# Kernel tuning notes

Hardware: AMD Instinct MI355X
Metric: run time of the kernel (lower is better)

Reference implementation:

```python
import jax, jax.numpy as jnp
import numpy as np

B, S, H, E, TOP_K = 4, 2048, 1024, 16, 4


def setup_inputs() -> dict:
    key = jax.random.key(0)
    ks = jax.random.split(key, 12)
    sc = 1.0 / np.sqrt(H)
    inp = {
        "x": jax.random.normal(ks[0], (B, S, H), dtype=jnp.float32),
        "image": jax.random.normal(ks[1], (B, S, H), dtype=jnp.float32),
        "text": jax.random.normal(ks[2], (B, S, H), dtype=jnp.float32),
        "audio": jax.random.normal(ks[3], (B, S, H), dtype=jnp.float32),
        # generalized router linear
        "Wg": jax.random.uniform(ks[4], (H, E), jnp.float32, -sc, sc),
        "bg": jax.random.uniform(ks[5], (E,), jnp.float32, -sc, sc),
        # per-modality router linears
        "Wi": jax.random.uniform(ks[6], (H, E), jnp.float32, -sc, sc),
        "bi": jax.random.uniform(ks[7], (E,), jnp.float32, -sc, sc),
        "Wt": jax.random.uniform(ks[8], (H, E), jnp.float32, -sc, sc),
        "bt": jax.random.uniform(ks[9], (E,), jnp.float32, -sc, sc),
        "Wa": jax.random.uniform(ks[10], (H, E), jnp.float32, -sc, sc),
        "ba": jax.random.uniform(ks[11], (E,), jnp.float32, -sc, sc),
    }
    return inp


def reference(x, image, text, audio, Wg, bg, Wi, bi, Wt, bt, Wa, ba):
    # combined_logits = generalized_router(x) + sum_m modality_router_m(modality_m)
    logits = (
        jnp.einsum("bsh,he->bse", x, Wg) + bg
        + jnp.einsum("bsh,he->bse", image, Wi) + bi
        + jnp.einsum("bsh,he->bse", text, Wt) + bt
        + jnp.einsum("bsh,he->bse", audio, Wa) + ba
    )  # [B,S,E]
    router_probs = jax.nn.softmax(logits, axis=-1)
    top_k_probs, top_k_indices = jax.lax.top_k(router_probs, TOP_K)
    top_k_probs = top_k_probs / jnp.sum(top_k_probs, axis=-1, keepdims=True)
    prob_per_expert = jnp.mean(router_probs, axis=(0, 1))  # [E]
    aux_loss = jnp.sum(prob_per_expert * jnp.log(prob_per_expert * E + 1e-9))
    return (top_k_indices, top_k_probs, aux_loss)
```

## Files before the change

kernel.cpp:

```cpp
#include <hip/hip_runtime.h>
#include <math.h>

constexpr int kTokens = 8192;
constexpr int kH      = 1024;
constexpr int kE      = 16;
constexpr int kTopK   = 4;
constexpr int kNC     = 16;

__global__ __launch_bounds__(128, 5)
void router_fmac(const float* __restrict__ x,   const float* __restrict__ img,
                 const float* __restrict__ txt, const float* __restrict__ aud,
                 const float* __restrict__ Wg,  const float* __restrict__ Wi,
                 const float* __restrict__ Wt,  const float* __restrict__ Wa,
                 float* __restrict__ partials)
{
    __shared__ float smem[2 * 2560];

    const int t   = threadIdx.x;
    const int bid = blockIdx.x;
    const int ks  = bid & 15;
    const int tg  = bid >> 4;
    const int m   = ks >> 2;
    const int k0  = (ks & 3) * 256;
    const int tok0 = tg * 128;

    const float* Xm = (m == 0) ? x  : (m == 1) ? img : (m == 2) ? txt : aud;
    const float* Wm = (m == 0) ? Wg : (m == 1) ? Wi  : (m == 2) ? Wt  : Wa;

    const int sc = t & 3;
    const int sr = t >> 2;

    float4 pf[4];

    {
        const float* src = Xm + (size_t)(tok0 + sr) * kH + k0 + sc * 4;
#pragma unroll
        for (int it = 0; it < 4; ++it)
            pf[it] = *(const float4*)(src + (size_t)(it * 32) * kH);
#pragma unroll
        for (int it = 0; it < 4; ++it)
            *(float4*)&smem[(sr + it * 32) * 20 + sc * 4] = pf[it];
    }
    __syncthreads();

    double dacc[kE];
#pragma unroll
    for (int e = 0; e < kE; ++e) dacc[e] = 0.0;
    float facc[kE];

    for (int p = 0; p < 16; ++p) {
        if (p < 15) {
            const float* src = Xm + (size_t)(tok0 + sr) * kH + k0 + (p + 1) * 16 + sc * 4;
#pragma unroll
            for (int it = 0; it < 4; ++it)
                pf[it] = *(const float4*)(src + (size_t)(it * 32) * kH);
        }

        if ((p & 3) == 0) {
#pragma unroll
            for (int e = 0; e < kE; ++e) facc[e] = 0.f;
        }

        const float* buf = smem + (p & 1) * 2560;
        float4 xv[4];
#pragma unroll
        for (int j4 = 0; j4 < 4; ++j4)
            xv[j4] = *(const float4*)&buf[t * 20 + j4 * 4];

        const float* wrow = Wm + (size_t)(k0 + p * 16) * kE;
#pragma unroll
        for (int j = 0; j < 16; ++j) {
            const float4 xq = xv[j >> 2];
            const int    jc = j & 3;
            const float  xh = (jc == 0) ? xq.x : (jc == 1) ? xq.y : (jc == 2) ? xq.z : xq.w;
            const float* wr = wrow + j * kE;
            const float4 w0 = *(const float4*)(wr + 0);
            const float4 w1 = *(const float4*)(wr + 4);
            const float4 w2 = *(const float4*)(wr + 8);
            const float4 w3 = *(const float4*)(wr + 12);
            facc[0]  += xh * w0.x;  facc[1]  += xh * w0.y;
            facc[2]  += xh * w0.z;  facc[3]  += xh * w0.w;
            facc[4]  += xh * w1.x;  facc[5]  += xh * w1.y;
            facc[6]  += xh * w1.z;  facc[7]  += xh * w1.w;
            facc[8]  += xh * w2.x;  facc[9]  += xh * w2.y;
            facc[10] += xh * w2.z;  facc[11] += xh * w2.w;
            facc[12] += xh * w3.x;  facc[13] += xh * w3.y;
            facc[14] += xh * w3.z;  facc[15] += xh * w3.w;
        }

        if ((p & 3) == 3) {
#pragma unroll
            for (int e = 0; e < kE; ++e) dacc[e] += (double)facc[e];
        }

        if (p < 15) {
            float* nb = smem + ((p + 1) & 1) * 2560;
#pragma unroll
            for (int it = 0; it < 4; ++it)
                *(float4*)&nb[(sr + it * 32) * 20 + sc * 4] = pf[it];
        }
        __syncthreads();
    }

    float* pp = partials + ((size_t)ks * kTokens + tok0 + t) * kE;
#pragma unroll
    for (int q = 0; q < 4; ++q) {
        *(float4*)&pp[q * 4] = make_float4((float)dacc[q * 4 + 0], (float)dacc[q * 4 + 1],
                                           (float)dacc[q * 4 + 2], (float)dacc[q * 4 + 3]);
    }
}

__global__ __launch_bounds__(256)
void router_topk(const float* __restrict__ partials,
                 const float* __restrict__ bg, const float* __restrict__ bi,
                 const float* __restrict__ bt, const float* __restrict__ ba,
                 float* __restrict__ out, float* __restrict__ blocksum)
{
    __shared__ double lgs[64][kE + 1];
    __shared__ float  pr[64][kE + 1];

    const int t    = threadIdx.x;
    const int tq   = t >> 2;
    const int eq   = t & 3;
    const int tok0 = blockIdx.x * 64;

    double a0 = (double)bg[eq*4+0] + (double)bi[eq*4+0] + (double)bt[eq*4+0] + (double)ba[eq*4+0];
    double a1 = (double)bg[eq*4+1] + (double)bi[eq*4+1] + (double)bt[eq*4+1] + (double)ba[eq*4+1];
    double a2 = (double)bg[eq*4+2] + (double)bi[eq*4+2] + (double)bt[eq*4+2] + (double)ba[eq*4+2];
    double a3 = (double)bg[eq*4+3] + (double)bi[eq*4+3] + (double)bt[eq*4+3] + (double)ba[eq*4+3];

#pragma unroll
    for (int c = 0; c < kNC; ++c) {
        const float4 v = *(const float4*)(partials + ((size_t)c * kTokens + tok0 + tq) * kE + eq * 4);
        a0 += (double)v.x;  a1 += (double)v.y;  a2 += (double)v.z;  a3 += (double)v.w;
    }
    lgs[tq][eq*4+0] = a0;  lgs[tq][eq*4+1] = a1;
    lgs[tq][eq*4+2] = a2;  lgs[tq][eq*4+3] = a3;
    __syncthreads();

    if (t < 64) {
        const int tok = tok0 + t;
        double lg[kE];
#pragma unroll
        for (int e = 0; e < kE; ++e) lg[e] = lgs[t][e];

        double mx = lg[0];
#pragma unroll
        for (int e = 1; e < kE; ++e) mx = fmax(mx, lg[e]);

        float p[kE];
        float sum = 0.f;
#pragma unroll
        for (int e = 0; e < kE; ++e) {
            p[e] = expf((float)(lg[e] - mx));
            sum += p[e];
        }
        const float inv = 1.f / sum;
#pragma unroll
        for (int e = 0; e < kE; ++e) { p[e] *= inv; pr[t][e] = p[e]; }

        unsigned used = 0;
        float tp[kTopK];
        int   ti[kTopK];
        float s4 = 0.f;
#pragma unroll
        for (int k = 0; k < kTopK; ++k) {
            float best = -1.f;
            int   bidx = 0;
#pragma unroll
            for (int e = 0; e < kE; ++e) {
                if (!((used >> e) & 1u) && p[e] > best) { best = p[e]; bidx = e; }
            }
            used |= 1u << bidx;
            tp[k] = best;
            ti[k] = bidx;
            s4 += best;
        }
        const float rn = 1.f / s4;

        *(float4*)&out[(size_t)tok * kTopK] =
            make_float4((float)ti[0], (float)ti[1], (float)ti[2], (float)ti[3]);
        *(float4*)&out[(size_t)kTokens * kTopK + (size_t)tok * kTopK] =
            make_float4(tp[0] * rn, tp[1] * rn, tp[2] * rn, tp[3] * rn);
    }
    __syncthreads();

    if (t < kE) {
        float s = 0.f;
#pragma unroll
        for (int tk = 0; tk < 64; ++tk) s += pr[tk][t];
        blocksum[blockIdx.x * kE + t] = s;
    }
}

__global__ __launch_bounds__(64)
void router_aux(const float* __restrict__ blocksum, float* __restrict__ out)
{
    __shared__ double ps[kE];
    const int t = threadIdx.x;
    if (t < kE) {
        double s = 0.0;
        for (int b = 0; b < 128; ++b) s += (double)blocksum[b * kE + t];
        ps[t] = s / (double)kTokens;
    }
    __syncthreads();
    if (t == 0) {
        double aux = 0.0;
#pragma unroll
        for (int e = 0; e < kE; ++e) aux += ps[e] * log(ps[e] * (double)kE + 1e-9);
        out[(size_t)kTokens * kTopK * 2] = (float)aux;
    }
}

extern "C" void kernel_launch(void* const* d_in, const int* in_sizes, int n_in,
                              void* d_out, int out_size, void* d_ws, size_t ws_size,
                              hipStream_t stream)
{
    const float* x   = (const float*)d_in[0];
    const float* img = (const float*)d_in[1];
    const float* txt = (const float*)d_in[2];
    const float* aud = (const float*)d_in[3];
    const float* Wg  = (const float*)d_in[4];
    const float* bg  = (const float*)d_in[5];
    const float* Wi  = (const float*)d_in[6];
    const float* bi  = (const float*)d_in[7];
    const float* Wt  = (const float*)d_in[8];
    const float* bt  = (const float*)d_in[9];
    const float* Wa  = (const float*)d_in[10];
    const float* ba  = (const float*)d_in[11];

    float* out      = (float*)d_out;
    float* partials = (float*)d_ws;
    float* blocksum = (float*)((char*)d_ws + (size_t)kNC * kTokens * kE * 4);

    router_fmac<<<1024, 128, 0, stream>>>(x, img, txt, aud, Wg, Wi, Wt, Wa, partials);
    router_topk<<<128, 256, 0, stream>>>(partials, bg, bi, bt, ba, out, blocksum);
    router_aux<<<1, 64, 0, stream>>>(blocksum, out);
}
```

Baseline: 201.3 us.

## Stage router weights in LDS and use 4x4 register tiles per thread

The fused router matmul kernel now loads each block's 256x16 weight slice into LDS once, instead of every thread reading weights from global memory. Each thread computes a 4-token by 4-expert tile rather than one token by all 16 experts. Blocks grow to 256 threads covering 256 tokens, and x is staged in 32-column chunks with a padded stride. This cuts global and L2 weight traffic and raises reuse of each x value, at the cost of more LDS, a second barrier per step and fewer blocks.

```diff
diff --git a/kernel.cpp b/kernel.cpp
--- a/kernel.cpp
+++ b/kernel.cpp
@@ -7,106 +7,120 @@
 constexpr int kTopK   = 4;
 constexpr int kNC     = 16;
 
-__global__ __launch_bounds__(128, 5)
+__global__ __launch_bounds__(256, 3)
 void router_fmac(const float* __restrict__ x,   const float* __restrict__ img,
                  const float* __restrict__ txt, const float* __restrict__ aud,
                  const float* __restrict__ Wg,  const float* __restrict__ Wi,
                  const float* __restrict__ Wt,  const float* __restrict__ Wa,
                  float* __restrict__ partials)
 {
-    __shared__ float smem[2 * 2560];
+    __shared__ float wlds[4096];
+    __shared__ float xlds[256 * 36];
 
     const int t   = threadIdx.x;
+    const int w   = t >> 6;
+    const int ln  = t & 63;
+    const int tq  = ln >> 2;
+    const int eq  = ln & 3;
     const int bid = blockIdx.x;
-    const int ks  = bid & 15;
-    const int tg  = bid >> 4;
+    const int ks  = bid >> 5;
+    const int tg  = bid & 31;
     const int m   = ks >> 2;
     const int k0  = (ks & 3) * 256;
-    const int tok0 = tg * 128;
+    const int tok0 = tg * 256;
 
     const float* Xm = (m == 0) ? x  : (m == 1) ? img : (m == 2) ? txt : aud;
     const float* Wm = (m == 0) ? Wg : (m == 1) ? Wi  : (m == 2) ? Wt  : Wa;
 
-    const int sc = t & 3;
-    const int sr = t >> 2;
-
-    float4 pf[4];
+    {
+        const float4* wsrc = (const float4*)(Wm + (size_t)k0 * kE);
+#pragma unroll
+        for (int i = 0; i < 4; ++i) {
+            const float4 v = wsrc[t + i * 256];
+            *(float4*)&wlds[(t + i * 256) * 4] = v;
+        }
+    }
+
+    const int sc = t & 7;
+    const int sr = t >> 3;
+    float4 pf[8];
 
     {
         const float* src = Xm + (size_t)(tok0 + sr) * kH + k0 + sc * 4;
 #pragma unroll
-        for (int it = 0; it < 4; ++it)
-            pf[it] = *(const float4*)(src + (size_t)(it * 32) * kH);
-#pragma unroll
-        for (int it = 0; it < 4; ++it)
-            *(float4*)&smem[(sr + it * 32) * 20 + sc * 4] = pf[it];
-    }
-    __syncthreads();
-
-    double dacc[kE];
-#pragma unroll
-    for (int e = 0; e < kE; ++e) dacc[e] = 0.0;
-    float facc[kE];
-
-    for (int p = 0; p < 16; ++p) {
-        if (p < 15) {
-            const float* src = Xm + (size_t)(tok0 + sr) * kH + k0 + (p + 1) * 16 + sc * 4;
-#pragma unroll
-            for (int it = 0; it < 4; ++it)
-                pf[it] = *(const float4*)(src + (size_t)(it * 32) * kH);
-        }
-
-        if ((p & 3) == 0) {
-#pragma unroll
-            for (int e = 0; e < kE; ++e) facc[e] = 0.f;
-        }
-
-        const float* buf = smem + (p & 1) * 2560;
-        float4 xv[4];
-#pragma unroll
-        for (int j4 = 0; j4 < 4; ++j4)
-            xv[j4] = *(const float4*)&buf[t * 20 + j4 * 4];
-
-        const float* wrow = Wm + (size_t)(k0 + p * 16) * kE;
-#pragma unroll
-        for (int j = 0; j < 16; ++j) {
-            const float4 xq = xv[j >> 2];
-            const int    jc = j & 3;
-            const float  xh = (jc == 0) ? xq.x : (jc == 1) ? xq.y : (jc == 2) ? xq.z : xq.w;
-            const float* wr = wrow + j * kE;
-            const float4 w0 = *(const float4*)(wr + 0);
-            const float4 w1 = *(const float4*)(wr + 4);
-            const float4 w2 = *(const float4*)(wr + 8);
-            const float4 w3 = *(const float4*)(wr + 12);
-            facc[0]  += xh * w0.x;  facc[1]  += xh * w0.y;
-            facc[2]  += xh * w0.z;  facc[3]  += xh * w0.w;
-            facc[4]  += xh * w1.x;  facc[5]  += xh * w1.y;
-            facc[6]  += xh * w1.z;  facc[7]  += xh * w1.w;
-            facc[8]  += xh * w2.x;  facc[9]  += xh * w2.y;
-            facc[10] += xh * w2.z;  facc[11] += xh * w2.w;
-            facc[12] += xh * w3.x;  facc[13] += xh * w3.y;
-            facc[14] += xh * w3.z;  facc[15] += xh * w3.w;
-        }
-
-        if ((p & 3) == 3) {
-#pragma unroll
-            for (int e = 0; e < kE; ++e) dacc[e] += (double)facc[e];
-        }
-
-        if (p < 15) {
-            float* nb = smem + ((p + 1) & 1) * 2560;
-#pragma unroll
-            for (int it = 0; it < 4; ++it)
-                *(float4*)&nb[(sr + it * 32) * 20 + sc * 4] = pf[it];
-        }
+        for (int i = 0; i < 8; ++i)
+            pf[i] = *(const float4*)(src + (size_t)(i * 32) * kH);
+#pragma unroll
+        for (int i = 0; i < 8; ++i)
+            *(float4*)&xlds[(sr + i * 32) * 36 + sc * 4] = pf[i];
+    }
+    __syncthreads();
+
+    float  facc[4][4];
+    double dacc[4][4];
+#pragma unroll
+    for (int i = 0; i < 4; ++i)
+#pragma unroll
+        for (int q = 0; q < 4; ++q) dacc[i][q] = 0.0;
+
+    const int r0 = w * 64 + tq;
+
+    for (int p = 0; p < 8; ++p) {
+        if (p < 7) {
+            const float* src = Xm + (size_t)(tok0 + sr) * kH + k0 + (p + 1) * 32 + sc * 4;
+#pragma unroll
+            for (int i = 0; i < 8; ++i)
+                pf[i] = *(const float4*)(src + (size_t)(i * 32) * kH);
+        }
+
+        if ((p & 1) == 0) {
+#pragma unroll
+            for (int i = 0; i < 4; ++i)
+#pragma unroll
+                for (int q = 0; q < 4; ++q) facc[i][q] = 0.f;
+        }
+
+#pragma unroll
+        for (int h4 = 0; h4 < 8; ++h4) {
+            float4 xv[4];
+#pragma unroll
+            for (int i = 0; i < 4; ++i)
+                xv[i] = *(const float4*)&xlds[(r0 + 16 * i) * 36 + h4 * 4];
+#pragma unroll
+            for (int j = 0; j < 4; ++j) {
+                const float4 wv = *(const float4*)&wlds[(p * 32 + h4 * 4 + j) * 16 + eq * 4];
+#pragma unroll
+                for (int i = 0; i < 4; ++i) {
+                    const float xh = (j == 0) ? xv[i].x : (j == 1) ? xv[i].y
+                                   : (j == 2) ? xv[i].z : xv[i].w;
+                    facc[i][0] += xh * wv.x;  facc[i][1] += xh * wv.y;
+                    facc[i][2] += xh * wv.z;  facc[i][3] += xh * wv.w;
+                }
+            }
+        }
+
+        if ((p & 1) == 1) {
+#pragma unroll
+            for (int i = 0; i < 4; ++i)
+#pragma unroll
+                for (int q = 0; q < 4; ++q) dacc[i][q] += (double)facc[i][q];
+        }
+
         __syncthreads();
-    }
-
-    float* pp = partials + ((size_t)ks * kTokens + tok0 + t) * kE;
-#pragma unroll
-    for (int q = 0; q < 4; ++q) {
-        *(float4*)&pp[q * 4] = make_float4((float)dacc[q * 4 + 0], (float)dacc[q * 4 + 1],
-                                           (float)dacc[q * 4 + 2], (float)dacc[q * 4 + 3]);
+        if (p < 7) {
+#pragma unroll
+            for (int i = 0; i < 8; ++i)
+                *(float4*)&xlds[(sr + i * 32) * 36 + sc * 4] = pf[i];
+        }
+        __syncthreads();
+    }
+
+#pragma unroll
+    for (int i = 0; i < 4; ++i) {
+        const int token = tok0 + w * 64 + tq + 16 * i;
+        *(float4*)&partials[((size_t)ks * kTokens + token) * kE + eq * 4] =
+            make_float4((float)dacc[i][0], (float)dacc[i][1],
+                        (float)dacc[i][2], (float)dacc[i][3]);
     }
 }
 
@@ -233,7 +247,7 @@
     float* partials = (float*)d_ws;
     float* blocksum = (float*)((char*)d_ws + (size_t)kNC * kTokens * kE * 4);
 
-    router_fmac<<<1024, 128, 0, stream>>>(x, img, txt, aud, Wg, Wi, Wt, Wa, partials);
+    router_fmac<<<512, 256, 0, stream>>>(x, img, txt, aud, Wg, Wi, Wt, Wa, partials);
     router_topk<<<128, 256, 0, stream>>>(partials, bg, bi, bt, ba, out, blocksum);
     router_aux<<<1, 64, 0, stream>>>(blocksum, out);
 }
```

Result: slower. 210.6 us (+4.6%).
